# Optimization experiments

Hardware: AMD Instinct MI355X
Metric: run time of the kernel (lower is better)

The kernel has to match this reference:

```python
import jax, jax.numpy as jnp
import numpy as np

TOP_K = 4
ALPHA = 1.702
LIMIT = 7.0


def _glu(x):
    # interleaved gate/up split, clamp, custom swiglu
    gate = x[..., ::2]
    up = x[..., 1::2]
    gate = jnp.minimum(gate, LIMIT)
    up = jnp.clip(up, -LIMIT, LIMIT)
    glu = gate * jax.nn.sigmoid(gate * ALPHA)
    return (up + 1.0) * glu


def setup_inputs() -> dict:
    key = jax.random.key(0)
    ks = jax.random.split(key, 7)
    B, S, H, F, E = 1, 1024, 2880, 2880, 16
    w_scale = 0.02
    return {
        "hidden_states": jax.random.normal(ks[0], (B, S, H), dtype=jnp.float32),
        "router_w": jax.random.normal(ks[1], (E, H), dtype=jnp.float32) * w_scale,
        "router_b": jax.random.normal(ks[2], (E,), dtype=jnp.float32) * w_scale,
        "gate_up_w": jax.random.normal(ks[3], (E, H, 2 * F), dtype=jnp.float32) * w_scale,
        "gate_up_b": jax.random.normal(ks[4], (E, 2 * F), dtype=jnp.float32) * w_scale,
        "down_w": jax.random.normal(ks[5], (E, F, H), dtype=jnp.float32) * w_scale,
        "down_b": jax.random.normal(ks[6], (E, H), dtype=jnp.float32) * w_scale,
    }


def reference(hidden_states, router_w, router_b, gate_up_w, gate_up_b, down_w, down_b):
    B, S, H = hidden_states.shape
    x = hidden_states.reshape(-1, H)  # [T, H]
    T = x.shape[0]

    # Router: linear + top-k + softmax over top-k values, scattered to full [T, E]
    logits = x @ router_w.T + router_b  # [T, E]
    top_v, top_i = jax.lax.top_k(logits, TOP_K)  # [T, K]
    top_v = jax.nn.softmax(top_v, axis=-1)  # normalized top-k affinities
    scores = jnp.zeros_like(logits).at[jnp.arange(T)[:, None], top_i].set(top_v)  # [T, E]

    # Expert GLU MLPs (dense over experts; zero affinity masks unselected experts)
    gu = jnp.einsum('th,ehf->etf', x, gate_up_w) + gate_up_b[:, None, :]  # [E, T, 2F]
    act = _glu(gu)  # [E, T, F]
    out_e = jnp.einsum('etf,efh->eth', act, down_w) + down_b[:, None, :]  # [E, T, H]

    # Combine weighted by router scores
    out = jnp.einsum('te,eth->th', scores, out_e)  # [T, H]
    return out.reshape(B, S, H)
```

## Files before the change

### kernel.cpp

```cpp
#include <hip/hip_runtime.h>
#include <hip/hip_bf16.h>
#include <math.h>

#define H_DIM 2880
#define F_DIM 2880
#define GU_DIM 5760
#define NE 16
#define NT 1024
#define TOPK 4

typedef float f32x4 __attribute__((ext_vector_type(4)));
typedef __bf16 bf16x8 __attribute__((ext_vector_type(8)));

__device__ __forceinline__ unsigned short f2bf(float f) {
    union { float f; unsigned u; } v; v.f = f;
    return (unsigned short)((v.u + 0x8000u) >> 16);
}
__device__ __forceinline__ unsigned pk2(float a, float b) {
    return (unsigned)f2bf(a) | ((unsigned)f2bf(b) << 16);
}

__global__ __launch_bounds__(64) void router_kernel(
    const float* __restrict__ x, const float* __restrict__ rw, const float* __restrict__ rb,
    int* counts, int* topk_idx, float* topk_score)
{
    int t = blockIdx.x, lane = threadIdx.x;
    const float* xr = x + (size_t)t * H_DIM;
    float acc[NE];
#pragma unroll
    for (int e = 0; e < NE; e++) acc[e] = 0.f;
    for (int h = lane; h < H_DIM; h += 64) {
        float xv = xr[h];
#pragma unroll
        for (int e = 0; e < NE; e++) acc[e] += xv * rw[e * H_DIM + h];
    }
    float lg[NE];
#pragma unroll
    for (int e = 0; e < NE; e++) {
        float v = acc[e];
#pragma unroll
        for (int off = 32; off > 0; off >>= 1) v += __shfl_down(v, off, 64);
        lg[e] = v;
    }
    if (lane == 0) {
#pragma unroll
        for (int e = 0; e < NE; e++) lg[e] += rb[e];
        int mask = 0; float tv[TOPK]; int ti[TOPK];
        for (int k = 0; k < TOPK; k++) {
            float best = -1e30f; int bi = 0;
            for (int e = 0; e < NE; e++)
                if (!((mask >> e) & 1) && lg[e] > best) { best = lg[e]; bi = e; }
            mask |= 1 << bi; tv[k] = best; ti[k] = bi;
        }
        float m = tv[0], s = 0.f, ex[TOPK];
        for (int k = 0; k < TOPK; k++) { ex[k] = expf(tv[k] - m); s += ex[k]; }
        float inv = 1.f / s;
        for (int k = 0; k < TOPK; k++) {
            topk_idx[t * TOPK + k] = ti[k];
            topk_score[t * TOPK + k] = ex[k] * inv;
            atomicAdd(&counts[ti[k]], 1);
        }
    }
}

__global__ void offsets_kernel(const int* counts, int* offsets) {
    if (threadIdx.x == 0 && blockIdx.x == 0) {
        int s = 0;
        for (int e = 0; e < NE; e++) { offsets[e] = s; s += counts[e]; }
        offsets[NE] = s;
    }
}

__global__ void scatter_kernel(const int* topk_idx, const float* topk_score,
                               const int* offsets, int* fills, int* entry, float* entry_score)
{
    int t = blockIdx.x * blockDim.x + threadIdx.x;
    if (t >= NT) return;
    for (int k = 0; k < TOPK; k++) {
        int e = topk_idx[t * TOPK + k];
        int pos = atomicAdd(&fills[e], 1);
        int i = offsets[e] + pos;
        entry[i] = t | (k << 16);
        entry_score[i] = topk_score[t * TOPK + k];
    }
}

__global__ __launch_bounds__(256, 2) void gemm1_kernel(
    const float* __restrict__ x, const float* __restrict__ gw, const float* __restrict__ gb,
    const int* __restrict__ counts, const int* __restrict__ offsets,
    const int* __restrict__ entry, unsigned short* __restrict__ act)
{
    int e = blockIdx.z;
    int cnt = counts[e];
    int m0 = blockIdx.y * 128;
    if (m0 >= cnt) return;
    int n0 = blockIdx.x * 128;
    int off = offsets[e];

    __shared__ __align__(16) unsigned short As[128 * 40];
    __shared__ __align__(16) unsigned short Bs[128 * 40];
    __shared__ int toks[128];

    int tid = threadIdx.x;
    if (tid < 128) {
        int r = m0 + tid;
        toks[tid] = entry[off + (r < cnt ? r : 0)] & 0xFFFF;
    }
    __syncthreads();

    int arow[4], akk[4]; const float* aptr[4];
#pragma unroll
    for (int i = 0; i < 4; i++) {
        int s = tid + i * 256;
        arow[i] = s >> 3; akk[i] = (s & 7) * 4;
        aptr[i] = x + (size_t)toks[arow[i]] * H_DIM + akk[i];
    }
    int n4 = tid & 31, kb = tid >> 5;
    const float* bptr = gw + (size_t)e * H_DIM * GU_DIM + (size_t)kb * 4 * GU_DIM + n0 + n4 * 4;

    int wv = tid >> 6, lane = tid & 63;
    int wm = (wv & 1) * 64, wn = (wv >> 1) * 64;
    int r16 = lane & 15, q = lane >> 4;

    f32x4 acc[4][4] = {};
    int a_rd[4], b_rd[4];
#pragma unroll
    for (int i = 0; i < 4; i++) {
        int m = wm + i * 16 + r16;
        a_rd[i] = m * 40 + q * 8;
        int n = wn + i * 16 + r16;
        b_rd[i] = n * 40 + ((q ^ ((n >> 2) & 3)) * 8);
    }
    int bwr[4];
#pragma unroll
    for (int c = 0; c < 4; c++) {
        int nl = n4 * 4 + c;
        bwr[c] = nl * 40 + (((kb >> 1) ^ ((nl >> 2) & 3)) * 8) + (kb & 1) * 4;
    }

    for (int k0 = 0; k0 < H_DIM; k0 += 32) {
#pragma unroll
        for (int i = 0; i < 4; i++) {
            float4 v = *(const float4*)(aptr[i] + k0);
            *(uint2*)&As[arow[i] * 40 + akk[i]] = make_uint2(pk2(v.x, v.y), pk2(v.z, v.w));
        }
        float bvf[4][4];
#pragma unroll
        for (int j = 0; j < 4; j++) {
            float4 tv = *(const float4*)(bptr + (size_t)(k0 + j) * GU_DIM);
            bvf[j][0] = tv.x; bvf[j][1] = tv.y; bvf[j][2] = tv.z; bvf[j][3] = tv.w;
        }
#pragma unroll
        for (int c = 0; c < 4; c++)
            *(uint2*)&Bs[bwr[c]] = make_uint2(pk2(bvf[0][c], bvf[1][c]), pk2(bvf[2][c], bvf[3][c]));
        __syncthreads();

        bf16x8 af[4], bq[4];
#pragma unroll
        for (int i = 0; i < 4; i++) af[i] = *(const bf16x8*)&As[a_rd[i]];
#pragma unroll
        for (int i = 0; i < 4; i++) bq[i] = *(const bf16x8*)&Bs[b_rd[i]];
#pragma unroll
        for (int mi = 0; mi < 4; mi++)
#pragma unroll
            for (int ni = 0; ni < 4; ni++)
                acc[mi][ni] = __builtin_amdgcn_mfma_f32_16x16x32_bf16(af[mi], bq[ni], acc[mi][ni], 0, 0, 0);
        __syncthreads();
    }

    const float* gbp = gb + (size_t)e * GU_DIM;
#pragma unroll
    for (int ni = 0; ni < 4; ni++) {
        int col = n0 + wn + ni * 16 + r16;
        float bias = gbp[col];
#pragma unroll
        for (int mi = 0; mi < 4; mi++) {
#pragma unroll
            for (int r = 0; r < 4; r++) {
                float v = acc[mi][ni][r] + bias;
                float vo = __shfl_xor(v, 1, 64);
                float gate = (lane & 1) ? vo : v;
                float up   = (lane & 1) ? v  : vo;
                gate = fminf(gate, 7.0f);
                up = fminf(fmaxf(up, -7.0f), 7.0f);
                float glu = gate / (1.0f + expf(-1.702f * gate));
                float a = (up + 1.0f) * glu;
                int row = m0 + wm + mi * 16 + q * 4 + r;
                if (row < cnt && !(lane & 1))
                    act[(size_t)(off + row) * F_DIM + (col >> 1)] = f2bf(a);
            }
        }
    }
}

__global__ __launch_bounds__(256, 2) void gemm2_kernel(
    const unsigned short* __restrict__ act, const float* __restrict__ dw, const float* __restrict__ db,
    const int* __restrict__ counts, const int* __restrict__ offsets,
    const int* __restrict__ entry, const float* __restrict__ entry_score,
    float* __restrict__ out)
{
    int e = blockIdx.z;
    int cnt = counts[e];
    int m0 = blockIdx.y * 128;
    if (m0 >= cnt) return;
    int n0 = blockIdx.x * 128;
    int off = offsets[e];

    __shared__ __align__(16) unsigned short As[128 * 40];
    __shared__ __align__(16) unsigned short Bs[128 * 40];
    __shared__ int tks[128];
    __shared__ float scs[128];

    int tid = threadIdx.x;
    if (tid < 128) {
        int r = m0 + tid;
        int idx = off + (r < cnt ? r : 0);
        tks[tid] = entry[idx];
        scs[tid] = entry_score[idx];
    }
    __syncthreads();

    int arow[2], ak8[2]; const unsigned short* aptr[2];
#pragma unroll
    for (int i = 0; i < 2; i++) {
        int s = tid + i * 256;
        arow[i] = s >> 2; ak8[i] = (s & 3) * 8;
        aptr[i] = act + (size_t)(off + m0 + arow[i]) * F_DIM + ak8[i];
    }
    int n4 = tid & 31, kb = tid >> 5;
    int ncol = n0 + n4 * 4;
    bool nval = ncol < H_DIM;
    const float* bptr = dw + (size_t)e * F_DIM * H_DIM + (size_t)kb * 4 * H_DIM + ncol;

    int wv = tid >> 6, lane = tid & 63;
    int wm = (wv & 1) * 64, wn = (wv >> 1) * 64;
    int r16 = lane & 15, q = lane >> 4;

    f32x4 acc[4][4] = {};
    int a_rd[4], b_rd[4];
#pragma unroll
    for (int i = 0; i < 4; i++) {
        int m = wm + i * 16 + r16;
        a_rd[i] = m * 40 + q * 8;
        int n = wn + i * 16 + r16;
        b_rd[i] = n * 40 + ((q ^ ((n >> 2) & 3)) * 8);
    }
    int bwr[4];
#pragma unroll
    for (int c = 0; c < 4; c++) {
        int nl = n4 * 4 + c;
        bwr[c] = nl * 40 + (((kb >> 1) ^ ((nl >> 2) & 3)) * 8) + (kb & 1) * 4;
    }

    for (int k0 = 0; k0 < F_DIM; k0 += 32) {
#pragma unroll
        for (int i = 0; i < 2; i++) {
            uint4 v = *(const uint4*)(aptr[i] + k0);
            *(uint4*)&As[arow[i] * 40 + ak8[i]] = v;
        }
        float bvf[4][4];
#pragma unroll
        for (int j = 0; j < 4; j++) {
            float4 tv = nval ? *(const float4*)(bptr + (size_t)(k0 + j) * H_DIM)
                             : make_float4(0.f, 0.f, 0.f, 0.f);
            bvf[j][0] = tv.x; bvf[j][1] = tv.y; bvf[j][2] = tv.z; bvf[j][3] = tv.w;
        }
#pragma unroll
        for (int c = 0; c < 4; c++)
            *(uint2*)&Bs[bwr[c]] = make_uint2(pk2(bvf[0][c], bvf[1][c]), pk2(bvf[2][c], bvf[3][c]));
        __syncthreads();

        bf16x8 af[4], bq[4];
#pragma unroll
        for (int i = 0; i < 4; i++) af[i] = *(const bf16x8*)&As[a_rd[i]];
#pragma unroll
        for (int i = 0; i < 4; i++) bq[i] = *(const bf16x8*)&Bs[b_rd[i]];
#pragma unroll
        for (int mi = 0; mi < 4; mi++)
#pragma unroll
            for (int ni = 0; ni < 4; ni++)
                acc[mi][ni] = __builtin_amdgcn_mfma_f32_16x16x32_bf16(af[mi], bq[ni], acc[mi][ni], 0, 0, 0);
        __syncthreads();
    }

    const float* dbp = db + (size_t)e * H_DIM;
#pragma unroll
    for (int ni = 0; ni < 4; ni++) {
        int col = n0 + wn + ni * 16 + r16;
        float bias = (col < H_DIM) ? dbp[col] : 0.f;
#pragma unroll
        for (int mi = 0; mi < 4; mi++) {
#pragma unroll
            for (int r = 0; r < 4; r++) {
                int lr = wm + mi * 16 + q * 4 + r;
                if (m0 + lr < cnt && col < H_DIM) {
                    int ev = tks[lr];
                    int tok = ev & 0xFFFF;
                    float v = (acc[mi][ni][r] + bias) * scs[lr];
                    atomicAdd(&out[(size_t)tok * H_DIM + col], v);
                }
            }
        }
    }
}

extern "C" void kernel_launch(void* const* d_in, const int* in_sizes, int n_in,
                              void* d_out, int out_size, void* d_ws, size_t ws_size,
                              hipStream_t stream)
{
    const float* x  = (const float*)d_in[0];
    const float* rw = (const float*)d_in[1];
    const float* rb = (const float*)d_in[2];
    const float* gw = (const float*)d_in[3];
    const float* gb = (const float*)d_in[4];
    const float* dw = (const float*)d_in[5];
    const float* db = (const float*)d_in[6];
    float* out = (float*)d_out;

    char* ws = (char*)d_ws;
    int*   counts      = (int*)(ws);
    int*   fills       = (int*)(ws + 64);
    int*   offsets     = (int*)(ws + 128);
    int*   topk_idx    = (int*)(ws + 256);
    float* topk_score  = (float*)(ws + 16640);
    int*   entry       = (int*)(ws + 33024);
    float* entry_score = (float*)(ws + 49408);
    unsigned short* act = (unsigned short*)(ws + 131072);

    hipMemsetAsync(ws, 0, 256, stream);
    hipMemsetAsync(d_out, 0, (size_t)out_size * 4, stream);

    router_kernel<<<NT, 64, 0, stream>>>(x, rw, rb, counts, topk_idx, topk_score);
    offsets_kernel<<<1, 32, 0, stream>>>(counts, offsets);
    scatter_kernel<<<4, 256, 0, stream>>>(topk_idx, topk_score, offsets, fills, entry, entry_score);
    gemm1_kernel<<<dim3(45, 8, NE), 256, 0, stream>>>(x, gw, gb, counts, offsets, entry, act);
    gemm2_kernel<<<dim3(23, 8, NE), 256, 0, stream>>>(act, dw, db, counts, offsets, entry, entry_score, out);
}
```

Measured before the change: 2.251 ms.

## Pre-cast x to bf16, load A tiles via global_load_lds, replace atomics with gather

A new kernel casts the hidden states to bf16 once, so gemm1 no longer converts fp32 activations on every tile load. Both GEMMs now stage their A tiles with direct global-to-LDS 16-byte loads into an XOR-swizzled 32-wide layout instead of going through registers. gemm2 writes per-slot weighted outputs to a workspace buffer, and a gather kernel sums each token's four slots, replacing the global float atomics and the output memset. This adds two kernel launches and about 47MB of extra workspace traffic. The direct-to-LDS loads are issued without an explicit vmcnt wait before the barrier, which could be a synchronisation hazard.

```diff
diff --git a/kernel.cpp b/kernel.cpp
--- a/kernel.cpp
+++ b/kernel.cpp
@@ -18,6 +18,24 @@
 }
 __device__ __forceinline__ unsigned pk2(float a, float b) {
     return (unsigned)f2bf(a) | ((unsigned)f2bf(b) << 16);
+}
+__device__ __forceinline__ void gload16(const void* gsrc, void* ldst) {
+    __builtin_amdgcn_global_load_lds(
+        (const __attribute__((address_space(1))) unsigned int*)gsrc,
+        (__attribute__((address_space(3))) unsigned int*)ldst,
+        16, 0, 0);
+}
+
+__global__ __launch_bounds__(256) void castx_kernel(const float* __restrict__ x,
+                                                    unsigned short* __restrict__ xb)
+{
+    int i = (blockIdx.x * 256 + threadIdx.x) * 8;
+    float4 a = *(const float4*)(x + i);
+    float4 b = *(const float4*)(x + i + 4);
+    uint4 o;
+    o.x = pk2(a.x, a.y); o.y = pk2(a.z, a.w);
+    o.z = pk2(b.x, b.y); o.w = pk2(b.z, b.w);
+    *(uint4*)(xb + i) = o;
 }
 
 __global__ __launch_bounds__(64) void router_kernel(
@@ -72,7 +90,8 @@
 }
 
 __global__ void scatter_kernel(const int* topk_idx, const float* topk_score,
-                               const int* offsets, int* fills, int* entry, float* entry_score)
+                               const int* offsets, int* fills, int* entry, float* entry_score,
+                               int* slot_map)
 {
     int t = blockIdx.x * blockDim.x + threadIdx.x;
     if (t >= NT) return;
@@ -82,11 +101,12 @@
         int i = offsets[e] + pos;
         entry[i] = t | (k << 16);
         entry_score[i] = topk_score[t * TOPK + k];
+        slot_map[t * TOPK + k] = i;
     }
 }
 
 __global__ __launch_bounds__(256, 2) void gemm1_kernel(
-    const float* __restrict__ x, const float* __restrict__ gw, const float* __restrict__ gb,
+    const unsigned short* __restrict__ xb, const float* __restrict__ gw, const float* __restrict__ gb,
     const int* __restrict__ counts, const int* __restrict__ offsets,
     const int* __restrict__ entry, unsigned short* __restrict__ act)
 {
@@ -97,7 +117,7 @@
     int n0 = blockIdx.x * 128;
     int off = offsets[e];
 
-    __shared__ __align__(16) unsigned short As[128 * 40];
+    __shared__ __align__(16) unsigned short As[128 * 32];
     __shared__ __align__(16) unsigned short Bs[128 * 40];
     __shared__ int toks[128];
 
@@ -108,17 +128,19 @@
     }
     __syncthreads();
 
-    int arow[4], akk[4]; const float* aptr[4];
-#pragma unroll
-    for (int i = 0; i < 4; i++) {
-        int s = tid + i * 256;
-        arow[i] = s >> 3; akk[i] = (s & 7) * 4;
-        aptr[i] = x + (size_t)toks[arow[i]] * H_DIM + akk[i];
-    }
+    int wv = tid >> 6, lane = tid & 63;
+
+    int ar0 = 32 * wv + (lane >> 2);
+    int ar1 = ar0 + 16;
+    int ac = lane & 3;
+    const unsigned short* asrc0 = xb + (size_t)toks[ar0] * H_DIM + 8 * (ac ^ ((ar0 >> 1) & 3));
+    const unsigned short* asrc1 = xb + (size_t)toks[ar1] * H_DIM + 8 * (ac ^ ((ar1 >> 1) & 3));
+    unsigned short* adst0 = &As[(32 * wv) * 32];
+    unsigned short* adst1 = &As[(32 * wv + 16) * 32];
+
     int n4 = tid & 31, kb = tid >> 5;
     const float* bptr = gw + (size_t)e * H_DIM * GU_DIM + (size_t)kb * 4 * GU_DIM + n0 + n4 * 4;
 
-    int wv = tid >> 6, lane = tid & 63;
     int wm = (wv & 1) * 64, wn = (wv >> 1) * 64;
     int r16 = lane & 15, q = lane >> 4;
 
@@ -127,7 +149,7 @@
 #pragma unroll
     for (int i = 0; i < 4; i++) {
         int m = wm + i * 16 + r16;
-        a_rd[i] = m * 40 + q * 8;
+        a_rd[i] = m * 32 + ((q ^ ((m >> 1) & 3)) * 8);
         int n = wn + i * 16 + r16;
         b_rd[i] = n * 40 + ((q ^ ((n >> 2) & 3)) * 8);
     }
@@ -139,11 +161,8 @@
     }
 
     for (int k0 = 0; k0 < H_DIM; k0 += 32) {
-#pragma unroll
-        for (int i = 0; i < 4; i++) {
-            float4 v = *(const float4*)(aptr[i] + k0);
-            *(uint2*)&As[arow[i] * 40 + akk[i]] = make_uint2(pk2(v.x, v.y), pk2(v.z, v.w));
-        }
+        gload16(asrc0 + k0, adst0);
+        gload16(asrc1 + k0, adst1);
         float bvf[4][4];
 #pragma unroll
         for (int j = 0; j < 4; j++) {
@@ -196,8 +215,7 @@
 __global__ __launch_bounds__(256, 2) void gemm2_kernel(
     const unsigned short* __restrict__ act, const float* __restrict__ dw, const float* __restrict__ db,
     const int* __restrict__ counts, const int* __restrict__ offsets,
-    const int* __restrict__ entry, const float* __restrict__ entry_score,
-    float* __restrict__ out)
+    const float* __restrict__ entry_score, float* __restrict__ slot_out)
 {
     int e = blockIdx.z;
     int cnt = counts[e];
@@ -206,33 +224,32 @@
     int n0 = blockIdx.x * 128;
     int off = offsets[e];
 
-    __shared__ __align__(16) unsigned short As[128 * 40];
+    __shared__ __align__(16) unsigned short As[128 * 32];
     __shared__ __align__(16) unsigned short Bs[128 * 40];
-    __shared__ int tks[128];
     __shared__ float scs[128];
 
     int tid = threadIdx.x;
     if (tid < 128) {
         int r = m0 + tid;
-        int idx = off + (r < cnt ? r : 0);
-        tks[tid] = entry[idx];
-        scs[tid] = entry_score[idx];
+        scs[tid] = entry_score[off + (r < cnt ? r : 0)];
     }
     __syncthreads();
 
-    int arow[2], ak8[2]; const unsigned short* aptr[2];
-#pragma unroll
-    for (int i = 0; i < 2; i++) {
-        int s = tid + i * 256;
-        arow[i] = s >> 2; ak8[i] = (s & 3) * 8;
-        aptr[i] = act + (size_t)(off + m0 + arow[i]) * F_DIM + ak8[i];
-    }
+    int wv = tid >> 6, lane = tid & 63;
+
+    int ar0 = 32 * wv + (lane >> 2);
+    int ar1 = ar0 + 16;
+    int ac = lane & 3;
+    const unsigned short* asrc0 = act + (size_t)(off + m0 + ar0) * F_DIM + 8 * (ac ^ ((ar0 >> 1) & 3));
+    const unsigned short* asrc1 = act + (size_t)(off + m0 + ar1) * F_DIM + 8 * (ac ^ ((ar1 >> 1) & 3));
+    unsigned short* adst0 = &As[(32 * wv) * 32];
+    unsigned short* adst1 = &As[(32 * wv + 16) * 32];
+
     int n4 = tid & 31, kb = tid >> 5;
     int ncol = n0 + n4 * 4;
     bool nval = ncol < H_DIM;
     const float* bptr = dw + (size_t)e * F_DIM * H_DIM + (size_t)kb * 4 * H_DIM + ncol;
 
-    int wv = tid >> 6, lane = tid & 63;
     int wm = (wv & 1) * 64, wn = (wv >> 1) * 64;
     int r16 = lane & 15, q = lane >> 4;
 
@@ -241,7 +258,7 @@
 #pragma unroll
     for (int i = 0; i < 4; i++) {
         int m = wm + i * 16 + r16;
-        a_rd[i] = m * 40 + q * 8;
+        a_rd[i] = m * 32 + ((q ^ ((m >> 1) & 3)) * 8);
         int n = wn + i * 16 + r16;
         b_rd[i] = n * 40 + ((q ^ ((n >> 2) & 3)) * 8);
     }
@@ -253,11 +270,8 @@
     }
 
     for (int k0 = 0; k0 < F_DIM; k0 += 32) {
-#pragma unroll
-        for (int i = 0; i < 2; i++) {
-            uint4 v = *(const uint4*)(aptr[i] + k0);
-            *(uint4*)&As[arow[i] * 40 + ak8[i]] = v;
-        }
+        gload16(asrc0 + k0, adst0);
+        gload16(asrc1 + k0, adst1);
         float bvf[4][4];
 #pragma unroll
         for (int j = 0; j < 4; j++) {
@@ -294,13 +308,32 @@
             for (int r = 0; r < 4; r++) {
                 int lr = wm + mi * 16 + q * 4 + r;
                 if (m0 + lr < cnt && col < H_DIM) {
-                    int ev = tks[lr];
-                    int tok = ev & 0xFFFF;
                     float v = (acc[mi][ni][r] + bias) * scs[lr];
-                    atomicAdd(&out[(size_t)tok * H_DIM + col], v);
+                    slot_out[(size_t)(off + m0 + lr) * H_DIM + col] = v;
                 }
             }
         }
+    }
+}
+
+__global__ __launch_bounds__(256) void gather_kernel(
+    const float* __restrict__ slot_out, const int* __restrict__ slot_map,
+    float* __restrict__ out)
+{
+    int t = blockIdx.x;
+    int s0 = slot_map[t * TOPK + 0];
+    int s1 = slot_map[t * TOPK + 1];
+    int s2 = slot_map[t * TOPK + 2];
+    int s3 = slot_map[t * TOPK + 3];
+    const float* r0 = slot_out + (size_t)s0 * H_DIM;
+    const float* r1 = slot_out + (size_t)s1 * H_DIM;
+    const float* r2 = slot_out + (size_t)s2 * H_DIM;
+    const float* r3 = slot_out + (size_t)s3 * H_DIM;
+    float* op = out + (size_t)t * H_DIM;
+    for (int h = threadIdx.x * 4; h < H_DIM; h += 1024) {
+        f32x4 v = *(const f32x4*)(r0 + h) + *(const f32x4*)(r1 + h)
+                + *(const f32x4*)(r2 + h) + *(const f32x4*)(r3 + h);
+        *(f32x4*)(op + h) = v;
     }
 }
 
@@ -325,14 +358,18 @@
     float* topk_score  = (float*)(ws + 16640);
     int*   entry       = (int*)(ws + 33024);
     float* entry_score = (float*)(ws + 49408);
+    int*   slot_map    = (int*)(ws + 65792);
     unsigned short* act = (unsigned short*)(ws + 131072);
+    unsigned short* xb  = (unsigned short*)(ws + 131072 + 24330240);
+    float* slot_out     = (float*)(ws + 30359552);
 
     hipMemsetAsync(ws, 0, 256, stream);
-    hipMemsetAsync(d_out, 0, (size_t)out_size * 4, stream);
-
+
+    castx_kernel<<<1440, 256, 0, stream>>>(x, xb);
     router_kernel<<<NT, 64, 0, stream>>>(x, rw, rb, counts, topk_idx, topk_score);
     offsets_kernel<<<1, 32, 0, stream>>>(counts, offsets);
-    scatter_kernel<<<4, 256, 0, stream>>>(topk_idx, topk_score, offsets, fills, entry, entry_score);
-    gemm1_kernel<<<dim3(45, 8, NE), 256, 0, stream>>>(x, gw, gb, counts, offsets, entry, act);
-    gemm2_kernel<<<dim3(23, 8, NE), 256, 0, stream>>>(act, dw, db, counts, offsets, entry, entry_score, out);
-}
+    scatter_kernel<<<4, 256, 0, stream>>>(topk_idx, topk_score, offsets, fills, entry, entry_score, slot_map);
+    gemm1_kernel<<<dim3(45, 8, NE), 256, 0, stream>>>(xb, gw, gb, counts, offsets, entry, act);
+    gemm2_kernel<<<dim3(23, 8, NE), 256, 0, stream>>>(act, dw, db, counts, offsets, entry_score, slot_out);
+    gather_kernel<<<NT, 256, 0, stream>>>(slot_out, slot_map, out);
+}
```

New measurement: 2.142 ms. 1.05x faster.
